# Kernel optimization log

Measured on AMD Instinct MI355X. Metric: run time of the kernel, lower is better.

## Reference

```python
import jax, jax.numpy as jnp
import numpy as np

D_MODEL = 1024
N_HEADS = 16
HEAD_DIM = D_MODEL // N_HEADS
THETA = 10000.0
B, S = 4, 2048


def setup_inputs() -> dict:
    key = jax.random.key(0)
    ks = jax.random.split(key, 5)
    scale = 1.0 / np.sqrt(D_MODEL)
    x = jax.random.normal(ks[0], (B, S, D_MODEL), dtype=jnp.float32)
    token_positions = jnp.broadcast_to(jnp.arange(S, dtype=jnp.int32)[None, :], (B, S))
    WQ = jax.random.normal(ks[1], (D_MODEL, D_MODEL), dtype=jnp.float32) * scale
    WK = jax.random.normal(ks[2], (D_MODEL, D_MODEL), dtype=jnp.float32) * scale
    WV = jax.random.normal(ks[3], (D_MODEL, D_MODEL), dtype=jnp.float32) * scale
    WO = jax.random.normal(ks[4], (D_MODEL, D_MODEL), dtype=jnp.float32) * scale
    return {"x": x, "token_positions": token_positions, "WQ": WQ, "WK": WK, "WV": WV, "WO": WO}


def _apply_rope(t, token_positions):
    # t: [b, h, s, d]; token_positions: [b, s]
    d = t.shape[-1]
    inv_freq = THETA ** (-jnp.arange(0, d, 2, dtype=jnp.float32) / d)  # [d/2]
    ang = token_positions.astype(jnp.float32)[:, None, :, None] * inv_freq  # [b,1,s,d/2]
    cos, sin = jnp.cos(ang), jnp.sin(ang)
    t_even, t_odd = t[..., 0::2], t[..., 1::2]
    r_even = t_even * cos - t_odd * sin
    r_odd = t_even * sin + t_odd * cos
    out = jnp.stack([r_even, r_odd], axis=-1)  # interleave pairs back
    return out.reshape(t.shape)


def reference(x, token_positions, WQ, WK, WV, WO):
    b, s, _ = x.shape
    def proj(W):
        y = jnp.einsum('bsd,ed->bse', x, W)  # Linear: x @ W^T, W is [out,in]
        return y.reshape(b, s, N_HEADS, HEAD_DIM).transpose(0, 2, 1, 3)  # [b,h,s,d]
    Q = _apply_rope(proj(WQ), token_positions)
    K = _apply_rope(proj(WK), token_positions)
    V = proj(WV)
    scores = jnp.einsum('bhqd,bhkd->bhqk', Q, K) / jnp.sqrt(jnp.float32(HEAD_DIM))
    causal = jnp.tril(jnp.ones((s, s), dtype=bool))
    scores = jnp.where(causal, scores, -jnp.inf)
    attn = jax.nn.softmax(scores, axis=-1)
    out = jnp.einsum('bhqk,bhkd->bhqd', attn, V)
    out = out.transpose(0, 2, 1, 3).reshape(b, s, D_MODEL)
    return jnp.einsum('bse,oe->bso', out, WO)
```

## Files before the change

### kernel.cpp

```cpp
#include <hip/hip_runtime.h>

typedef __bf16 bf16x8 __attribute__((ext_vector_type(8)));
typedef __bf16 bf16x2 __attribute__((ext_vector_type(2)));
typedef float f32x4 __attribute__((ext_vector_type(4)));
typedef float f32x2 __attribute__((ext_vector_type(2)));
typedef unsigned short u16;
typedef unsigned int u32;

#define MFMA16(a, b, c) __builtin_amdgcn_mfma_f32_16x16x32_bf16((a), (b), (c), 0, 0, 0)

__device__ __forceinline__ u16 f2b(float f) {
  u32 u = __float_as_uint(f);
  u += 0x7FFFu + ((u >> 16) & 1u);
  return (u16)(u >> 16);
}
__device__ __forceinline__ float b2f(u16 h) { return __uint_as_float(((u32)h) << 16); }

__device__ __forceinline__ u32 pkbf(float a, float b) {
  bf16x2 h = {(__bf16)a, (__bf16)b};
  return __builtin_bit_cast(u32, h);
}

__device__ __forceinline__ float max3f(float a, float b, float c) {
  float d;
  asm("v_max3_f32 %0, %1, %2, %3" : "=v"(d) : "v"(a), "v"(b), "v"(c));
  return d;
}

__device__ __forceinline__ float exp2_(float x) {
#if __has_builtin(__builtin_amdgcn_exp2f)
  return __builtin_amdgcn_exp2f(x);
#else
  return exp2f(x);
#endif
}

__device__ __forceinline__ void glds16(const void* g, void* l) {
  __builtin_amdgcn_global_load_lds((const __attribute__((address_space(1))) void*)g,
                                   (__attribute__((address_space(3))) void*)l, 16, 0, 0);
}

__global__ __launch_bounds__(256) void cvt_k(const float* __restrict__ x,
                                             const float* __restrict__ wq,
                                             const float* __restrict__ wk,
                                             const float* __restrict__ wv,
                                             const float* __restrict__ wo,
                                             u16* __restrict__ dst) {
  size_t e = ((size_t)blockIdx.x * 256 + threadIdx.x) * 4;
  const float* src;
  size_t off;
  if (e < 8388608ull) {
    src = x; off = e;
  } else {
    size_t r = e - 8388608ull;
    u32 wi = (u32)(r >> 20);
    off = r & 1048575ull;
    src = (wi == 0) ? wq : (wi == 1) ? wk : (wi == 2) ? wv : wo;
  }
  float4 v = *(const float4*)(src + off);
  ushort4 o = make_ushort4(f2b(v.x), f2b(v.y), f2b(v.z), f2b(v.w));
  *(ushort4*)(dst + e) = o;
}

__global__ __launch_bounds__(256) void rope_tab_k(const int* __restrict__ pos,
                                                  float2* __restrict__ tab) {
  int i = blockIdx.x * 256 + threadIdx.x;
  int row = i >> 5, j = i & 31;
  float p = (float)pos[row];
  float inv = exp2f((float)j * -0.41524101186092029f);
  float s, c;
  sincosf(p * inv, &s, &c);
  tab[i] = make_float2(c, s);
}

__global__ __launch_bounds__(256, 3) void gemm_qkv_k(const u16* __restrict__ Xb,
                                                     const u16* __restrict__ Wq,
                                                     const u16* __restrict__ Wk,
                                                     const u16* __restrict__ Wv,
                                                     const float2* __restrict__ tab,
                                                     u16* __restrict__ Qp,
                                                     u16* __restrict__ Kp,
                                                     u16* __restrict__ Vt) {
  __shared__ u16 As[3][4096];
  __shared__ u16 Bs[3][4096];
  const int wgid = blockIdx.x;
  const int xcd = wgid & 7;
  const int idx = wgid >> 3;
  const int P = xcd * 24 + (idx >> 3);
  const int nt = idx & 7;
  const int z = P >> 6;
  const int mt = P & 63;
  const u16* W = (z == 0) ? Wq : (z == 1) ? Wk : Wv;
  const int t = threadIdx.x;
  const int wave = t >> 6, lane = t & 63;
  const int lr = lane & 15, lg = lane >> 4;
  const int wr = wave >> 1, wc = wave & 1;

  const int rr0 = t >> 3;
  const int s8 = t & 7;
  const int sl8 = s8 ^ (rr0 & 7);
  const int js = sl8 >> 2;
  const int kcs = sl8 & 3;
  const u16* aS = Xb + (size_t)(mt * 128 + rr0 + 64 * js) * 1024 + kcs * 8;
  const u16* bS = W + (size_t)(nt * 128 + rr0 + 64 * js) * 1024 + kcs * 8;

  f32x4 acc[4][4];
#pragma unroll
  for (int i = 0; i < 4; ++i)
#pragma unroll
    for (int j = 0; j < 4; ++j) acc[i][j] = (f32x4){0.f, 0.f, 0.f, 0.f};

#pragma unroll
  for (int tt = 0; tt < 2; ++tt) {
    const int kcol = tt * 32;
    glds16(aS + kcol, &As[tt][t * 8]);
    glds16(aS + 32 * 1024 + kcol, &As[tt][2048 + t * 8]);
    glds16(bS + kcol, &Bs[tt][t * 8]);
    glds16(bS + 32 * 1024 + kcol, &Bs[tt][2048 + t * 8]);
  }
  asm volatile("s_waitcnt vmcnt(4)" ::: "memory");
  __builtin_amdgcn_s_barrier();

  const int arb = lr * 64 + (((wr << 2) + lg) ^ (lr & 7)) * 8;
  const int brb = lr * 64 + (((wc << 2) + lg) ^ (lr & 7)) * 8;

  int sl = 0, sp2 = 2;
  for (int tau = 0; tau < 32; ++tau) {
    const u16* Asl = &As[sl][0];
    const u16* Bsl = &Bs[sl][0];
    bf16x8 af[4], bf[4];
#pragma unroll
    for (int mi = 0; mi < 4; ++mi) af[mi] = *(const bf16x8*)&Asl[arb + mi * 1024];
#pragma unroll
    for (int nj = 0; nj < 4; ++nj) bf[nj] = *(const bf16x8*)&Bsl[brb + nj * 1024];
    if (tau < 30) {
      u16* Ad = &As[sp2][0];
      u16* Bd = &Bs[sp2][0];
      const int kcol = (tau + 2) * 32;
      glds16(aS + kcol, &Ad[t * 8]);
      glds16(aS + 32 * 1024 + kcol, &Ad[2048 + t * 8]);
      glds16(bS + kcol, &Bd[t * 8]);
      glds16(bS + 32 * 1024 + kcol, &Bd[2048 + t * 8]);
    }
    asm volatile("s_waitcnt lgkmcnt(0)" ::: "memory");
    __builtin_amdgcn_sched_barrier(0);
    __builtin_amdgcn_s_setprio(1);
#pragma unroll
    for (int mi = 0; mi < 4; ++mi)
#pragma unroll
      for (int nj = 0; nj < 4; ++nj)
        acc[mi][nj] = MFMA16(af[mi], bf[nj], acc[mi][nj]);
    __builtin_amdgcn_s_setprio(0);
    __builtin_amdgcn_sched_barrier(0);
    if (tau < 30) asm volatile("s_waitcnt vmcnt(4)" ::: "memory");
    else asm volatile("s_waitcnt vmcnt(0)" ::: "memory");
    __builtin_amdgcn_s_barrier();
    sl = (sl == 2) ? 0 : sl + 1;
    sp2 = (sp2 == 2) ? 0 : sp2 + 1;
  }

  const int rbase = mt * 128 + wr * 64 + lg * 4;
  const int cbase = nt * 128 + wc * 64 + lr;
  if (z < 2) {
    u16* out = (z == 0) ? Qp : Kp;
    const float scl = (z == 0) ? 0.18033688011112043f : 1.0f;
#pragma unroll
    for (int mi = 0; mi < 4; ++mi)
#pragma unroll
      for (int nj = 0; nj < 4; ++nj) {
        int row0 = rbase + mi * 16;
        int col = cbase + nj * 16;
        int j = (col >> 1) & 31;
        float sgn = (col & 1) ? 1.f : -1.f;
#pragma unroll
        for (int r = 0; r < 4; ++r) {
          float self = acc[mi][nj][r];
          float partner = __shfl_xor(self, 1);
          float2 cs = tab[(size_t)(row0 + r) * 32 + j];
          float o = (self * cs.x + partner * cs.y * sgn) * scl;
          out[(size_t)(row0 + r) * 1024 + col] = f2b(o);
        }
      }
  } else {
#pragma unroll
    for (int mi = 0; mi < 4; ++mi)
#pragma unroll
      for (int nj = 0; nj < 4; ++nj) {
        int row0 = rbase + mi * 16;
        int e = cbase + nj * 16;
        int b = row0 >> 11, s = row0 & 2047;
        ushort4 pk = make_ushort4(f2b(acc[mi][nj][0]), f2b(acc[mi][nj][1]),
                                  f2b(acc[mi][nj][2]), f2b(acc[mi][nj][3]));
        *(ushort4*)&Vt[((size_t)(b * 1024 + e)) * 2048 + s] = pk;
      }
  }
}

__global__ __launch_bounds__(512, 6) void fattn_k(const u16* __restrict__ Qp,
                                                  const u16* __restrict__ Kp,
                                                  const u16* __restrict__ Vt,
                                                  u16* __restrict__ Ao) {
  __shared__ u16 Ks[2][64 * 64];
  __shared__ u16 Vs[2][64 * 64];
  __shared__ u16 Ps[8][16 * 64];
  const int blk = blockIdx.x;
  const int g = blk & 7, jj = blk >> 3;
  const int bh = g * 8 + (jj & 7);
  const int qt = 15 - (jj >> 3);
  const int b = bh >> 4, h = bh & 15;
  const int tid = threadIdx.x, wave = tid >> 6, lane = tid & 63;
  const int lr = lane & 15, lg = lane >> 4;
  const int q0w = qt * 128 + wave * 16;

  bf16x8 qf0, qf1;
  {
    const u16* qb = Qp + ((size_t)(b * 2048 + q0w + lr)) * 1024 + h * 64 + lg * 8;
    qf0 = *(const bf16x8*)qb;
    qf1 = *(const bf16x8*)(qb + 32);
  }

  float m = -1e30f, l = 0.f;
  f32x4 oacc[4];
#pragma unroll
  for (int d4 = 0; d4 < 4; ++d4) oacc[d4] = (f32x4){0.f, 0.f, 0.f, 0.f};
  const f32x4 fz = {0.f, 0.f, 0.f, 0.f};

  const int srow = lane >> 3;
  const int schunk = (lane & 7) ^ srow;
  const u16* kbase = Kp + ((size_t)(b * 2048 + 8 * wave + srow)) * 1024 + h * 64 + schunk * 8;
  const u16* vbase = Vt + ((size_t)(b * 1024 + h * 64 + 8 * wave + srow)) * 2048 + schunk * 8;
  char* psbase = (char*)&Ps[wave][0];

  const int ktmax = 2 * qt + 1;
  const int ktneed = 2 * qt + (wave >> 2);

  glds16(kbase, &Ks[0][(8 * wave) * 64]);
  glds16(vbase, &Vs[0][(8 * wave) * 64]);

  int cur = 0;
  for (int kt = 0; kt <= ktmax; ++kt, cur ^= 1) {
    __syncthreads();
    if (kt < ktmax) {
      const int nx = cur ^ 1, k1 = kt + 1;
      glds16(kbase + (size_t)k1 * 65536, &Ks[nx][(8 * wave) * 64]);
      glds16(vbase + k1 * 64, &Vs[nx][(8 * wave) * 64]);
    }
    if (kt > ktneed) continue;
    const u16* KB = &Ks[cur][0];
    const u16* VB = &Vs[cur][0];

    f32x4 sc[4];
#pragma unroll
    for (int ks = 0; ks < 4; ++ks) {
      const int krow = ks * 16 + lr;
      const int swk = lr & 7;
      bf16x8 kf0 = *(const bf16x8*)&KB[krow * 64 + ((lg ^ swk) * 8)];
      bf16x8 kf1 = *(const bf16x8*)&KB[krow * 64 + (((lg + 4) ^ swk) * 8)];
      f32x4 s = MFMA16(kf0, qf0, fz);
      s = MFMA16(kf1, qf1, s);
      sc[ks] = s;
    }
    if (kt == ktneed) {
      int q = q0w + lr;
#pragma unroll
      for (int ks = 0; ks < 4; ++ks)
#pragma unroll
        for (int r = 0; r < 4; ++r) {
          int kv = kt * 64 + ks * 16 + lg * 4 + r;
          if (kv > q) sc[ks][r] = -__builtin_inff();
        }
    }

    {
      float t0 = max3f(sc[0][0], sc[0][1], sc[0][2]);
      float t1 = max3f(sc[0][3], sc[1][0], sc[1][1]);
      float t2 = max3f(sc[1][2], sc[1][3], sc[2][0]);
      float t3 = max3f(sc[2][1], sc[2][2], sc[2][3]);
      float t4 = max3f(sc[3][0], sc[3][1], sc[3][2]);
      float pm = max3f(max3f(t0, t1, t2), max3f(t3, t4, sc[3][3]), -1e30f);
      pm = fmaxf(pm, __shfl_xor(pm, 16));
      pm = fmaxf(pm, __shfl_xor(pm, 32));
      if (__any(pm > m + 8.f)) {
        float mn = fmaxf(m, pm);
        float corr = exp2_(m - mn);
        m = mn;
        l *= corr;
        float cb[4];
#pragma unroll
        for (int r = 0; r < 4; ++r) cb[r] = __shfl(corr, (lane & 48) | (lg * 4 + r));
#pragma unroll
        for (int d4 = 0; d4 < 4; ++d4)
#pragma unroll
          for (int r = 0; r < 4; ++r) oacc[d4][r] *= cb[r];
      }
      const f32x2 ms = {m, m};
      f32x2 rs2 = {0.f, 0.f};
#pragma unroll
      for (int ks = 0; ks < 4; ++ks) {
        f32x2 lo = {sc[ks][0], sc[ks][1]};
        f32x2 hi = {sc[ks][2], sc[ks][3]};
        lo = lo - ms;
        hi = hi - ms;
        lo[0] = exp2_(lo[0]); lo[1] = exp2_(lo[1]);
        hi[0] = exp2_(hi[0]); hi[1] = exp2_(hi[1]);
        rs2 += lo;
        rs2 += hi;
        sc[ks][0] = lo[0]; sc[ks][1] = lo[1];
        sc[ks][2] = hi[0]; sc[ks][3] = hi[1];
      }
      float rs = rs2[0] + rs2[1];
      rs += __shfl_xor(rs, 16);
      rs += __shfl_xor(rs, 32);
      l += rs;
    }

    bf16x8 pa0, pa1;
    {
      const int swp = lr & 7;
#pragma unroll
      for (int ks = 0; ks < 4; ++ks) {
        const int chunk = (2 * ks + (lg >> 1)) ^ swp;
        char* p = psbase + lr * 128 + chunk * 16 + (lg & 1) * 8;
        *(uint2*)p = make_uint2(pkbf(sc[ks][0], sc[ks][1]),
                                pkbf(sc[ks][2], sc[ks][3]));
      }
      pa0 = *(const bf16x8*)(psbase + lr * 128 + ((lg ^ swp) * 16));
      pa1 = *(const bf16x8*)(psbase + lr * 128 + (((lg + 4) ^ swp) * 16));
    }
#pragma unroll
    for (int d4 = 0; d4 < 4; ++d4) {
      const int vrow = d4 * 16 + lr;
      const int swv = lr & 7;
      bf16x8 vf0 = *(const bf16x8*)&VB[vrow * 64 + ((lg ^ swv) * 8)];
      bf16x8 vf1 = *(const bf16x8*)&VB[vrow * 64 + (((lg + 4) ^ swv) * 8)];
      oacc[d4] = MFMA16(pa0, vf0, oacc[d4]);
      oacc[d4] = MFMA16(pa1, vf1, oacc[d4]);
    }
  }

  {
    float lb[4];
#pragma unroll
    for (int r = 0; r < 4; ++r) lb[r] = __shfl(l, (lane & 48) | (lg * 4 + r));
#pragma unroll
    for (int r = 0; r < 4; ++r) {
      float inv = 1.f / lb[r];
      int q = q0w + lg * 4 + r;
      u16* orow = Ao + ((size_t)(b * 2048 + q)) * 1024 + h * 64 + lr;
#pragma unroll
      for (int d4 = 0; d4 < 4; ++d4) orow[d4 * 16] = f2b(oacc[d4][r] * inv);
    }
  }
}

__global__ __launch_bounds__(512, 2) void gemm_wo_k(const u16* __restrict__ Ab,
                                                    const u16* __restrict__ Wo,
                                                    float* __restrict__ Out) {
  __shared__ u16 As[3][16384];
  __shared__ u16 Bs[3][8192];
  const int wgid = blockIdx.x;
  const int xcd = wgid & 7;
  const int idx = wgid >> 3;
  const int mt = xcd * 4 + (idx >> 3);
  const int nt = idx & 7;
  const int t = threadIdx.x;
  const int wave = t >> 6, lane = t & 63;
  const int lr = lane & 15, lg = lane >> 4;
  const int wr = wave >> 1, wc = wave & 1;

  const int srow = t >> 3;
  const int scc = t & 7;
  const int ssw = scc ^ (srow & 7);
  const u16* aA = Ab + (size_t)(mt * 256 + srow) * 1024 + ssw * 8;
  const u16* bB = Wo + (size_t)(nt * 128 + srow) * 1024 + ssw * 8;

  f32x4 acc[4][4];
#pragma unroll
  for (int i = 0; i < 4; ++i)
#pragma unroll
    for (int j = 0; j < 4; ++j) acc[i][j] = (f32x4){0.f, 0.f, 0.f, 0.f};

#pragma unroll
  for (int tt = 0; tt < 2; ++tt) {
    const int kt = tt * 64;
    glds16(aA + kt, &As[tt][t * 8]);
    glds16(aA + 64 * 1024 + kt, &As[tt][4096 + t * 8]);
    glds16(bB + kt, &Bs[tt][t * 8]);
    glds16(aA + 128 * 1024 + kt, &As[tt][8192 + t * 8]);
    glds16(aA + 192 * 1024 + kt, &As[tt][12288 + t * 8]);
    glds16(bB + 64 * 1024 + kt, &Bs[tt][4096 + t * 8]);
  }
  asm volatile("s_waitcnt vmcnt(6)" ::: "memory");
  __builtin_amdgcn_s_barrier();

  const int arow = (wr * 64 + lr) * 64;
  const int brow = (wc * 64 + lr) * 64;
  const int sw = lr & 7;

  int sl = 0;
  for (int tau = 0; tau < 16; ++tau) {
    const int sp2 = (sl + 2 >= 3) ? sl - 1 : sl + 2;
    const u16* Asl = &As[sl][0];
    const u16* Bsl = &Bs[sl][0];
    u16* Ad = &As[sp2][0];
    u16* Bd = &Bs[sp2][0];
    const int kt2 = (tau + 2) * 64;
    bf16x8 af[4], bf[4];

    {
      const int koff = (lg ^ sw) * 8;
#pragma unroll
      for (int mi = 0; mi < 4; ++mi)
        af[mi] = *(const bf16x8*)&Asl[arow + mi * 1024 + koff];
#pragma unroll
      for (int nj = 0; nj < 4; ++nj)
        bf[nj] = *(const bf16x8*)&Bsl[brow + nj * 1024 + koff];
    }
    if (tau < 14) {
      glds16(aA + kt2, &Ad[t * 8]);
      glds16(aA + 64 * 1024 + kt2, &Ad[4096 + t * 8]);
      glds16(bB + kt2, &Bd[t * 8]);
    }
    __builtin_amdgcn_s_barrier();
    asm volatile("s_waitcnt lgkmcnt(0)" ::: "memory");
    __builtin_amdgcn_sched_barrier(0);
    __builtin_amdgcn_s_setprio(1);
#pragma unroll
    for (int mi = 0; mi < 4; ++mi)
#pragma unroll
      for (int nj = 0; nj < 4; ++nj)
        acc[mi][nj] = MFMA16(af[mi], bf[nj], acc[mi][nj]);
    __builtin_amdgcn_s_setprio(0);
    __builtin_amdgcn_sched_barrier(0);
    __builtin_amdgcn_s_barrier();

    {
      const int koff = ((4 + lg) ^ sw) * 8;
#pragma unroll
      for (int mi = 0; mi < 4; ++mi)
        af[mi] = *(const bf16x8*)&Asl[arow + mi * 1024 + koff];
#pragma unroll
      for (int nj = 0; nj < 4; ++nj)
        bf[nj] = *(const bf16x8*)&Bsl[brow + nj * 1024 + koff];
    }
    if (tau < 14) {
      glds16(aA + 128 * 1024 + kt2, &Ad[8192 + t * 8]);
      glds16(aA + 192 * 1024 + kt2, &Ad[12288 + t * 8]);
      glds16(bB + 64 * 1024 + kt2, &Bd[4096 + t * 8]);
    }
    __builtin_amdgcn_s_barrier();
    asm volatile("s_waitcnt lgkmcnt(0)" ::: "memory");
    __builtin_amdgcn_sched_barrier(0);
    __builtin_amdgcn_s_setprio(1);
#pragma unroll
    for (int mi = 0; mi < 4; ++mi)
#pragma unroll
      for (int nj = 0; nj < 4; ++nj)
        acc[mi][nj] = MFMA16(af[mi], bf[nj], acc[mi][nj]);
    __builtin_amdgcn_s_setprio(0);
    __builtin_amdgcn_sched_barrier(0);
    if (tau < 14) asm volatile("s_waitcnt vmcnt(6)" ::: "memory");
    else asm volatile("s_waitcnt vmcnt(0)" ::: "memory");
    __builtin_amdgcn_s_barrier();
    sl = (sl == 2) ? 0 : sl + 1;
  }

  const int rbase = mt * 256 + wr * 64 + lg * 4;
  const int cbase = nt * 128 + wc * 64 + lr;
#pragma unroll
  for (int mi = 0; mi < 4; ++mi)
#pragma unroll
    for (int nj = 0; nj < 4; ++nj) {
      int row0 = rbase + mi * 16;
      int col = cbase + nj * 16;
#pragma unroll
      for (int r = 0; r < 4; ++r)
        Out[(size_t)(row0 + r) * 1024 + col] = acc[mi][nj][r];
    }
}

extern "C" void kernel_launch(void* const* d_in, const int* in_sizes, int n_in,
                              void* d_out, int out_size, void* d_ws, size_t ws_size,
                              hipStream_t stream) {
  const float* x = (const float*)d_in[0];
  const int* pos = (const int*)d_in[1];
  const float* wq = (const float*)d_in[2];
  const float* wk = (const float*)d_in[3];
  const float* wv = (const float*)d_in[4];
  const float* wo = (const float*)d_in[5];

  char* ws = (char*)d_ws;
  u16* xb = (u16*)ws;
  u16* wqb = xb + 8388608;
  u16* wkb = wqb + 1048576;
  u16* wvb = wkb + 1048576;
  u16* wob = wvb + 1048576;
  float2* tab = (float2*)(ws + 25165824);
  u16* Qp = (u16*)(ws + 27262976);
  u16* Kp = (u16*)(ws + 27262976 + 16777216);
  u16* Vt = (u16*)(ws + 27262976 + 2 * 16777216);
  u16* Ao = (u16*)(ws + 27262976 + 3 * 16777216);

  hipLaunchKernelGGL(cvt_k, dim3(12288), dim3(256), 0, stream, x, wq, wk, wv, wo, xb);
  hipLaunchKernelGGL(rope_tab_k, dim3(1024), dim3(256), 0, stream, pos, tab);
  hipLaunchKernelGGL(gemm_qkv_k, dim3(1536), dim3(256), 0, stream, xb, wqb, wkb, wvb,
                     tab, Qp, Kp, Vt);
  hipLaunchKernelGGL(fattn_k, dim3(1024), dim3(512), 0, stream, Qp, Kp, Vt, Ao);
  hipLaunchKernelGGL(gemm_wo_k, dim3(256), dim3(512), 0, stream, Ao, wob, (float*)d_out);
}
```

Baseline: 162.7 us.

## Fuse rope table into convert kernel and retile output projection GEMM

The rope sin/cos table computation moves into the first 1024 blocks of the conversion kernel, which removes one kernel launch. The output projection GEMM is retiled from 256x128 tiles with 512 threads to 128x128 tiles with 256 threads and a K step of 32. Its grid grows from 256 to 512 workgroups, which fills more CUs on the 256-CU part, and it now has one barrier stage per iteration. The trade-off is less reuse per tile and more loop iterations with more barriers.

```diff
diff --git a/kernel.cpp b/kernel.cpp
--- a/kernel.cpp
+++ b/kernel.cpp
@@ -45,7 +45,9 @@
                                              const float* __restrict__ wk,
                                              const float* __restrict__ wv,
                                              const float* __restrict__ wo,
-                                             u16* __restrict__ dst) {
+                                             const int* __restrict__ pos,
+                                             u16* __restrict__ dst,
+                                             float2* __restrict__ tab) {
   size_t e = ((size_t)blockIdx.x * 256 + threadIdx.x) * 4;
   const float* src;
   size_t off;
@@ -60,17 +62,15 @@
   float4 v = *(const float4*)(src + off);
   ushort4 o = make_ushort4(f2b(v.x), f2b(v.y), f2b(v.z), f2b(v.w));
   *(ushort4*)(dst + e) = o;
-}
-
-__global__ __launch_bounds__(256) void rope_tab_k(const int* __restrict__ pos,
-                                                  float2* __restrict__ tab) {
-  int i = blockIdx.x * 256 + threadIdx.x;
-  int row = i >> 5, j = i & 31;
-  float p = (float)pos[row];
-  float inv = exp2f((float)j * -0.41524101186092029f);
-  float s, c;
-  sincosf(p * inv, &s, &c);
-  tab[i] = make_float2(c, s);
+  if (blockIdx.x < 1024) {
+    int i = blockIdx.x * 256 + threadIdx.x;
+    int row = i >> 5, j = i & 31;
+    float p = (float)pos[row];
+    float inv = exp2f((float)j * -0.41524101186092029f);
+    float s, c;
+    sincosf(p * inv, &s, &c);
+    tab[i] = make_float2(c, s);
+  }
 }
 
 __global__ __launch_bounds__(256, 3) void gemm_qkv_k(const u16* __restrict__ Xb,
@@ -353,26 +353,28 @@
   }
 }
 
-__global__ __launch_bounds__(512, 2) void gemm_wo_k(const u16* __restrict__ Ab,
+__global__ __launch_bounds__(256, 3) void gemm_wo_k(const u16* __restrict__ Ab,
                                                     const u16* __restrict__ Wo,
                                                     float* __restrict__ Out) {
-  __shared__ u16 As[3][16384];
-  __shared__ u16 Bs[3][8192];
+  __shared__ u16 As[3][4096];
+  __shared__ u16 Bs[3][4096];
   const int wgid = blockIdx.x;
   const int xcd = wgid & 7;
   const int idx = wgid >> 3;
-  const int mt = xcd * 4 + (idx >> 3);
+  const int mt = xcd * 8 + (idx >> 3);
   const int nt = idx & 7;
   const int t = threadIdx.x;
   const int wave = t >> 6, lane = t & 63;
   const int lr = lane & 15, lg = lane >> 4;
   const int wr = wave >> 1, wc = wave & 1;
 
-  const int srow = t >> 3;
-  const int scc = t & 7;
-  const int ssw = scc ^ (srow & 7);
-  const u16* aA = Ab + (size_t)(mt * 256 + srow) * 1024 + ssw * 8;
-  const u16* bB = Wo + (size_t)(nt * 128 + srow) * 1024 + ssw * 8;
+  const int rr0 = t >> 3;
+  const int s8 = t & 7;
+  const int sl8 = s8 ^ (rr0 & 7);
+  const int js = sl8 >> 2;
+  const int kcs = sl8 & 3;
+  const u16* aS = Ab + (size_t)(mt * 128 + rr0 + 64 * js) * 1024 + kcs * 8;
+  const u16* bS = Wo + (size_t)(nt * 128 + rr0 + 64 * js) * 1024 + kcs * 8;
 
   f32x4 acc[4][4];
 #pragma unroll
@@ -382,46 +384,36 @@
 
 #pragma unroll
   for (int tt = 0; tt < 2; ++tt) {
-    const int kt = tt * 64;
-    glds16(aA + kt, &As[tt][t * 8]);
-    glds16(aA + 64 * 1024 + kt, &As[tt][4096 + t * 8]);
-    glds16(bB + kt, &Bs[tt][t * 8]);
-    glds16(aA + 128 * 1024 + kt, &As[tt][8192 + t * 8]);
-    glds16(aA + 192 * 1024 + kt, &As[tt][12288 + t * 8]);
-    glds16(bB + 64 * 1024 + kt, &Bs[tt][4096 + t * 8]);
-  }
-  asm volatile("s_waitcnt vmcnt(6)" ::: "memory");
+    const int kcol = tt * 32;
+    glds16(aS + kcol, &As[tt][t * 8]);
+    glds16(aS + 32 * 1024 + kcol, &As[tt][2048 + t * 8]);
+    glds16(bS + kcol, &Bs[tt][t * 8]);
+    glds16(bS + 32 * 1024 + kcol, &Bs[tt][2048 + t * 8]);
+  }
+  asm volatile("s_waitcnt vmcnt(4)" ::: "memory");
   __builtin_amdgcn_s_barrier();
 
-  const int arow = (wr * 64 + lr) * 64;
-  const int brow = (wc * 64 + lr) * 64;
-  const int sw = lr & 7;
-
-  int sl = 0;
-  for (int tau = 0; tau < 16; ++tau) {
-    const int sp2 = (sl + 2 >= 3) ? sl - 1 : sl + 2;
+  const int arb = lr * 64 + (((wr << 2) + lg) ^ (lr & 7)) * 8;
+  const int brb = lr * 64 + (((wc << 2) + lg) ^ (lr & 7)) * 8;
+
+  int sl = 0, sp2 = 2;
+  for (int tau = 0; tau < 32; ++tau) {
     const u16* Asl = &As[sl][0];
     const u16* Bsl = &Bs[sl][0];
-    u16* Ad = &As[sp2][0];
-    u16* Bd = &Bs[sp2][0];
-    const int kt2 = (tau + 2) * 64;
     bf16x8 af[4], bf[4];
-
-    {
-      const int koff = (lg ^ sw) * 8;
-#pragma unroll
-      for (int mi = 0; mi < 4; ++mi)
-        af[mi] = *(const bf16x8*)&Asl[arow + mi * 1024 + koff];
-#pragma unroll
-      for (int nj = 0; nj < 4; ++nj)
-        bf[nj] = *(const bf16x8*)&Bsl[brow + nj * 1024 + koff];
-    }
-    if (tau < 14) {
-      glds16(aA + kt2, &Ad[t * 8]);
-      glds16(aA + 64 * 1024 + kt2, &Ad[4096 + t * 8]);
-      glds16(bB + kt2, &Bd[t * 8]);
-    }
-    __builtin_amdgcn_s_barrier();
+#pragma unroll
+    for (int mi = 0; mi < 4; ++mi) af[mi] = *(const bf16x8*)&Asl[arb + mi * 1024];
+#pragma unroll
+    for (int nj = 0; nj < 4; ++nj) bf[nj] = *(const bf16x8*)&Bsl[brb + nj * 1024];
+    if (tau < 30) {
+      u16* Ad = &As[sp2][0];
+      u16* Bd = &Bs[sp2][0];
+      const int kcol = (tau + 2) * 32;
+      glds16(aS + kcol, &Ad[t * 8]);
+      glds16(aS + 32 * 1024 + kcol, &Ad[2048 + t * 8]);
+      glds16(bS + kcol, &Bd[t * 8]);
+      glds16(bS + 32 * 1024 + kcol, &Bd[2048 + t * 8]);
+    }
     asm volatile("s_waitcnt lgkmcnt(0)" ::: "memory");
     __builtin_amdgcn_sched_barrier(0);
     __builtin_amdgcn_s_setprio(1);
@@ -432,40 +424,14 @@
         acc[mi][nj] = MFMA16(af[mi], bf[nj], acc[mi][nj]);
     __builtin_amdgcn_s_setprio(0);
     __builtin_amdgcn_sched_barrier(0);
-    __builtin_amdgcn_s_barrier();
-
-    {
-      const int koff = ((4 + lg) ^ sw) * 8;
-#pragma unroll
-      for (int mi = 0; mi < 4; ++mi)
-        af[mi] = *(const bf16x8*)&Asl[arow + mi * 1024 + koff];
-#pragma unroll
-      for (int nj = 0; nj < 4; ++nj)
-        bf[nj] = *(const bf16x8*)&Bsl[brow + nj * 1024 + koff];
-    }
-    if (tau < 14) {
-      glds16(aA + 128 * 1024 + kt2, &Ad[8192 + t * 8]);
-      glds16(aA + 192 * 1024 + kt2, &Ad[12288 + t * 8]);
-      glds16(bB + 64 * 1024 + kt2, &Bd[4096 + t * 8]);
-    }
-    __builtin_amdgcn_s_barrier();
-    asm volatile("s_waitcnt lgkmcnt(0)" ::: "memory");
-    __builtin_amdgcn_sched_barrier(0);
-    __builtin_amdgcn_s_setprio(1);
-#pragma unroll
-    for (int mi = 0; mi < 4; ++mi)
-#pragma unroll
-      for (int nj = 0; nj < 4; ++nj)
-        acc[mi][nj] = MFMA16(af[mi], bf[nj], acc[mi][nj]);
-    __builtin_amdgcn_s_setprio(0);
-    __builtin_amdgcn_sched_barrier(0);
-    if (tau < 14) asm volatile("s_waitcnt vmcnt(6)" ::: "memory");
+    if (tau < 30) asm volatile("s_waitcnt vmcnt(4)" ::: "memory");
     else asm volatile("s_waitcnt vmcnt(0)" ::: "memory");
     __builtin_amdgcn_s_barrier();
     sl = (sl == 2) ? 0 : sl + 1;
-  }
-
-  const int rbase = mt * 256 + wr * 64 + lg * 4;
+    sp2 = (sp2 == 2) ? 0 : sp2 + 1;
+  }
+
+  const int rbase = mt * 128 + wr * 64 + lg * 4;
   const int cbase = nt * 128 + wc * 64 + lr;
 #pragma unroll
   for (int mi = 0; mi < 4; ++mi)
@@ -501,10 +467,10 @@
   u16* Vt = (u16*)(ws + 27262976 + 2 * 16777216);
   u16* Ao = (u16*)(ws + 27262976 + 3 * 16777216);
 
-  hipLaunchKernelGGL(cvt_k, dim3(12288), dim3(256), 0, stream, x, wq, wk, wv, wo, xb);
-  hipLaunchKernelGGL(rope_tab_k, dim3(1024), dim3(256), 0, stream, pos, tab);
+  hipLaunchKernelGGL(cvt_k, dim3(12288), dim3(256), 0, stream, x, wq, wk, wv, wo, pos,
+                     xb, tab);
   hipLaunchKernelGGL(gemm_qkv_k, dim3(1536), dim3(256), 0, stream, xb, wqb, wkb, wvb,
                      tab, Qp, Kp, Vt);
   hipLaunchKernelGGL(fattn_k, dim3(1024), dim3(512), 0, stream, Qp, Kp, Vt, Ao);
-  hipLaunchKernelGGL(gemm_wo_k, dim3(256), dim3(512), 0, stream, Ao, wob, (float*)d_out);
-}
+  hipLaunchKernelGGL(gemm_wo_k, dim3(512), dim3(256), 0, stream, Ao, wob, (float*)d_out);
+}
```

New measurement: 161.6 us. Within noise of the previous version (-0.7%).
